# Optimization experiments

Measured on AMD Instinct MI355X. Metric: run time of the kernel, lower is better.

The kernel has to match this reference:

```python
import jax, jax.numpy as jnp
import numpy as np

T, B, E, H, F = 1024, 2, 1024, 16, 8
D = E // H
R = 2 * T - 1  # relative positions T-1 .. -(T-1)


def setup_inputs() -> dict:
    key = jax.random.key(0)
    ks = jax.random.split(key, 11)
    std = float(np.sqrt(2.0 / (E + E)))
    return {
        "input": jax.random.normal(ks[0], (T, B, E), jnp.float32),
        "pos": jax.random.normal(ks[1], (R, B, E), jnp.float32),
        "factor": jax.random.normal(ks[2], (F,), jnp.float32),
        "in_proj_weight": jax.random.normal(ks[3], (3 * E * E, F), jnp.float32) * std,
        "pos_proj_weight": jax.random.normal(ks[4], (E * E, F), jnp.float32) * std,
        "out_proj_weight": jax.random.normal(ks[5], (E * E, F), jnp.float32) * std,
        "in_proj_bias": jax.random.normal(ks[6], (3 * E, F), jnp.float32) * 0.02,
        "pos_proj_bias": jax.random.normal(ks[7], (E, F), jnp.float32) * 0.02,
        "out_proj_bias": jax.random.normal(ks[8], (E, F), jnp.float32) * 0.02,
        "r_w_bias": jax.random.normal(ks[9], (E, F), jnp.float32) * 0.02,
        "r_r_bias": jax.random.normal(ks[10], (E, F), jnp.float32) * 0.02,
    }


def _rel_shift(x):
    # x: [BH, T, R] -> out[b, i, j] = x[b, i, j + (T-1) - i]
    bh, q, r = x.shape
    zp = jnp.zeros((bh, q, 1), x.dtype)
    xp = jnp.concatenate([zp, x], axis=2).reshape(bh, r + 1, q)
    return xp[:, 1:, :].reshape(bh, q, r)


def reference(input, pos, factor, in_proj_weight, pos_proj_weight, out_proj_weight,
              in_proj_bias, pos_proj_bias, out_proj_bias, r_w_bias, r_r_bias):
    # hypernetwork: generate effective weights from factor vector (torch.mv)
    W_in = (in_proj_weight @ factor).reshape(3 * E, E)
    W_pos = (pos_proj_weight @ factor).reshape(E, E)
    W_out = (out_proj_weight @ factor).reshape(E, E)
    b_in = in_proj_bias @ factor
    b_pos = pos_proj_bias @ factor
    b_out = out_proj_bias @ factor
    rw = (r_w_bias @ factor).reshape(H, D)  # content bias
    rr = (r_r_bias @ factor).reshape(H, D)  # position bias

    qkv = input @ W_in.T + b_in                      # [T, B, 3E]
    q, k, v = jnp.split(qkv, 3, axis=-1)
    q = q.reshape(T, B, H, D)
    k = k.reshape(T, B, H, D)
    v = v.reshape(T, B, H, D)
    r = (pos @ W_pos.T + b_pos).reshape(R, B, H, D)  # [R, B, H, D]

    scale = 1.0 / np.sqrt(D)
    # AC: content-content + content bias term
    AC = jnp.einsum('ibhd,jbhd->bhij', q + rw, k)    # [B, H, T, T]
    # BD: content-position + position bias term, then relative shift
    BD = jnp.einsum('ibhd,rbhd->bhir', q + rr, r)    # [B, H, T, R]
    BD = _rel_shift(BD.reshape(B * H, T, R))[:, :, :T].reshape(B, H, T, T)

    attn = jax.nn.softmax((AC + BD) * scale, axis=-1)  # [B, H, T, T]
    out = jnp.einsum('bhij,jbhd->ibhd', attn, v).reshape(T, B, E)
    out = out @ W_out.T + b_out                       # [T, B, E]
    return out
```

## Files before the change

kernel.cpp:

```cpp
#include <hip/hip_runtime.h>


typedef _Float16 h16;
typedef _Float16 h16x8 __attribute__((ext_vector_type(8)));
typedef _Float16 h16x4 __attribute__((ext_vector_type(4)));
typedef float f32x4 __attribute__((ext_vector_type(4)));

static __device__ __forceinline__ f32x4 mfma16(h16x8 a, h16x8 b, f32x4 c) {
  return __builtin_amdgcn_mfma_f32_16x16x32_f16(a, b, c, 0, 0, 0);
}
static __device__ __forceinline__ void gload16(const void* g, void* l) {
  __builtin_amdgcn_global_load_lds((const __attribute__((address_space(1))) void*)g,
                                   (__attribute__((address_space(3))) void*)l, 16, 0, 0);
}

__global__ __launch_bounds__(256) void hypernet_kernel(
    const float* __restrict__ fac,
    const float* __restrict__ w_in, const float* __restrict__ w_pos,
    const float* __restrict__ w_out, const float* __restrict__ b_in_w,
    const float* __restrict__ b_pos_w, const float* __restrict__ b_out_w,
    const float* __restrict__ rw_w, const float* __restrict__ rr_w,
    h16* __restrict__ Win, h16* __restrict__ Wpos, h16* __restrict__ Wout,
    float* __restrict__ bin, float* __restrict__ bpos, float* __restrict__ bout,
    float* __restrict__ rw, float* __restrict__ rr, h16* __restrict__ rb,
    const float* __restrict__ input, h16* __restrict__ in_h,
    const float* __restrict__ pos, h16* __restrict__ pos_h)
{
  float f0=fac[0],f1=fac[1],f2=fac[2],f3=fac[3],f4=fac[4],f5=fac[5],f6=fac[6],f7=fac[7];
#define DOT8(p) ((p)[0]*f0+(p)[1]*f1+(p)[2]*f2+(p)[3]*f3+(p)[4]*f4+(p)[5]*f5+(p)[6]*f6+(p)[7]*f7)
  if (blockIdx.x < 5120) {
    const int lane = threadIdx.x & 63;
    const int gw = blockIdx.x * 4 + (threadIdx.x >> 6);
    size_t rowBase = (size_t)gw * 256;
    const float* srcp; h16* dstp; size_t lr;
    if (rowBase < 3145728)      { srcp = w_in;  dstp = Win;  lr = rowBase; }
    else if (rowBase < 4194304) { srcp = w_pos; dstp = Wpos; lr = rowBase - 3145728; }
    else                        { srcp = w_out; dstp = Wout; lr = rowBase - 4194304; }
    const f32x4* p = reinterpret_cast<const f32x4*>(srcp) + lr*2;
    const int pi = (lane < 32) ? (lane << 1) : (((lane - 32) << 1) | 1);
    const float fa = (lane < 32) ? f0 : f4;
    const float fb = (lane < 32) ? f1 : f5;
    const float fc = (lane < 32) ? f2 : f6;
    const float fd = (lane < 32) ? f3 : f7;
    f32x4 v[8];
#pragma unroll
    for (int u = 0; u < 8; ++u) v[u] = p[(size_t)u*64 + pi];
    __builtin_amdgcn_sched_barrier(0);
    float full[8];
#pragma unroll
    for (int u = 0; u < 8; ++u) {
      float part = v[u].x*fa + v[u].y*fb + v[u].z*fc + v[u].w*fd;
      full[u] = part + __shfl_xor(part, 32, 64);
    }
    if (lane < 32) {
#pragma unroll
      for (int u = 0; u < 8; ++u)
        dstp[lr + u*32 + lane] = (h16)full[u];
    }
    return;
  }
  int idx = (blockIdx.x - 5120) * 256 + threadIdx.x;
  if (idx < 3072) { bin[idx]  = DOT8(b_in_w  + (size_t)idx*8); return; }
  idx -= 3072;
  if (idx < 1024) { bpos[idx] = DOT8(b_pos_w + (size_t)idx*8); return; }
  idx -= 1024;
  if (idx < 1024) { bout[idx] = DOT8(b_out_w + (size_t)idx*8); return; }
  idx -= 1024;
  if (idx < 1024) { rw[idx]   = DOT8(rw_w    + (size_t)idx*8); return; }
  idx -= 1024;
  if (idx < 1024) { rr[idx]   = DOT8(rr_w    + (size_t)idx*8); return; }
  idx -= 1024;
  if (idx < 2048) { rb[(((size_t)(idx >> 6)) << 17) + 2047*64 + (idx & 63)] = (h16)0.f; return; }
  idx -= 2048;
  if (idx < 262144) {
    const float4* ip = reinterpret_cast<const float4*>(input) + (size_t)idx*2;
    float4 a = ip[0], b = ip[1];
    h16x8 o = { (h16)a.x, (h16)a.y, (h16)a.z, (h16)a.w,
                (h16)b.x, (h16)b.y, (h16)b.z, (h16)b.w };
    reinterpret_cast<h16x8*>(in_h)[idx] = o;
    return;
  }
  idx -= 262144;
  if (idx < 524032) {
    const float4* pp = reinterpret_cast<const float4*>(pos) + (size_t)idx*2;
    float4 a = pp[0], b = pp[1];
    h16x8 o = { (h16)a.x, (h16)a.y, (h16)a.z, (h16)a.w,
                (h16)b.x, (h16)b.y, (h16)b.z, (h16)b.w };
    reinterpret_cast<h16x8*>(pos_h)[idx] = o;
  }
#undef DOT8
}

__global__ __launch_bounds__(256) void gemm01_kernel(
    const h16* __restrict__ A0, const h16* __restrict__ B0, const float* __restrict__ bias0,
    const h16* __restrict__ A1, const h16* __restrict__ B1, const float* __restrict__ bias1,
    const float* __restrict__ rwv, const float* __restrict__ rrv,
    h16* __restrict__ o0, h16* __restrict__ o1,
    h16* __restrict__ o2, h16* __restrict__ o3, h16* __restrict__ r_out)
{
  __shared__ __align__(16) h16 a_sm[128*64];
  __shared__ __align__(16) h16 b_sm[128*64];
  const int bx = blockIdx.x;
  const int swz = (bx & 7) * 80 + (bx >> 3);
  int mode, bxx, byy;
  if (swz < 384) { mode = 0; bxx = swz % 24; byy = swz / 24; }
  else           { mode = 1; int b = swz - 384; bxx = b & 7; byy = b >> 3; }
  const h16* __restrict__ A  = mode ? A1 : A0;
  const h16* __restrict__ Bw = mode ? B1 : B0;
  const float* __restrict__ bias = mode ? bias1 : bias0;
  const int M = mode ? 4094 : 2048;
  const int K = 1024;

  const int tid = threadIdx.x, lane = tid & 63, wave = tid >> 6;
  const int quad = lane >> 4, t16 = lane & 15;
  const int wm = wave >> 1, wn = wave & 1;
  const int m0 = byy * 128, n0 = bxx * 128;
  const int lrow = lane >> 3, lgran = lane & 7;
  const int gsw = (lgran ^ lrow) * 8;
  const int xg0 = (quad ^ (t16 & 7)) * 8;
  const int xg1 = xg0 ^ 32;

  f32x4 acc[4][4];
#pragma unroll
  for (int i = 0; i < 4; ++i)
#pragma unroll
    for (int j = 0; j < 4; ++j) acc[i][j] = (f32x4){0.f,0.f,0.f,0.f};

  for (int k0 = 0; k0 < K; k0 += 64) {
    __syncthreads();
#pragma unroll
    for (int s = 0; s < 4; ++s) {
      int rbase = wave*32 + s*8;
      gload16(A  + (size_t)(m0 + rbase + lrow)*K + k0 + gsw, a_sm + rbase*64);
      gload16(Bw + (size_t)(n0 + rbase + lrow)*K + k0 + gsw, b_sm + rbase*64);
    }
    __syncthreads();
#pragma unroll
    for (int kc = 0; kc < 2; ++kc) {
      const int xg = kc ? xg1 : xg0;
      h16x8 af[4], bfr[4];
#pragma unroll
      for (int i = 0; i < 4; ++i) {
        af[i]  = *reinterpret_cast<const h16x8*>(a_sm + (wm*64 + i*16 + t16)*64 + xg);
        bfr[i] = *reinterpret_cast<const h16x8*>(b_sm + (wn*64 + i*16 + t16)*64 + xg);
      }
#pragma unroll
      for (int i = 0; i < 4; ++i)
#pragma unroll
        for (int j = 0; j < 4; ++j)
          acc[i][j] = mfma16(af[i], bfr[j], acc[i][j]);
    }
  }

#pragma unroll
  for (int i = 0; i < 4; ++i) {
    int mb = m0 + wm*64 + i*16 + quad*4;
#pragma unroll
    for (int j = 0; j < 4; ++j) {
      int n = n0 + wn*64 + j*16 + t16;
      float bv = bias[n];
      if (mode == 0) {
        int nn = n & 1023, sec = n >> 10, hh = nn >> 6, d = nn & 63;
        float rwb = rwv[nn], rrb = rrv[nn];
#pragma unroll
        for (int r = 0; r < 4; ++r) {
          int m = mb + r, t = m >> 1, b = m & 1;
          size_t off = ((size_t)((b << 4) + hh) << 16) + (t << 6) + d;
          float v = acc[i][j][r] + bv;
          if (sec == 0)      { o0[off] = (h16)(v + rwb); o1[off] = (h16)(v + rrb); }
          else if (sec == 1) { o2[off] = (h16)v; }
          else               { o3[off] = (h16)v; }
        }
      } else {
        int hh = n >> 6, d = n & 63;
#pragma unroll
        for (int r = 0; r < 4; ++r) {
          int m = mb + r;
          if (m < M) {
            int rel = m >> 1, b = m & 1;
            r_out[(((size_t)((b << 4) + hh)) << 17) + (rel << 6) + d] = (h16)(acc[i][j][r] + bv);
          }
        }
      }
    }
  }
}

template <int MODE>
__global__ __launch_bounds__(256) void gemm_lds_kernel(
    const h16* __restrict__ A, const h16* __restrict__ Bw,
    const float* __restrict__ bias, int M, int N, int K,
    float* __restrict__ Cout)
{
  __shared__ __align__(16) h16 a_sm[128*64];
  __shared__ __align__(16) h16 b_sm[128*64];
  const int tid = threadIdx.x, lane = tid & 63, wave = tid >> 6;
  const int quad = lane >> 4, t16 = lane & 15;
  const int wm = wave >> 1, wn = wave & 1;
  const int m0 = blockIdx.y * 128, n0 = blockIdx.x * 128;
  const int lrow = lane >> 3, lgran = lane & 7;
  const int gsw = (lgran ^ lrow) * 8;
  const int xg0 = (quad ^ (t16 & 7)) * 8;
  const int xg1 = xg0 ^ 32;

  f32x4 acc[4][4];
#pragma unroll
  for (int i = 0; i < 4; ++i)
#pragma unroll
    for (int j = 0; j < 4; ++j) acc[i][j] = (f32x4){0.f,0.f,0.f,0.f};

  for (int k0 = 0; k0 < K; k0 += 64) {
    __syncthreads();
#pragma unroll
    for (int s = 0; s < 4; ++s) {
      int rbase = wave*32 + s*8;
      gload16(A  + (size_t)(m0 + rbase + lrow)*K + k0 + gsw, a_sm + rbase*64);
      gload16(Bw + (size_t)(n0 + rbase + lrow)*K + k0 + gsw, b_sm + rbase*64);
    }
    __syncthreads();
#pragma unroll
    for (int kc = 0; kc < 2; ++kc) {
      const int xg = kc ? xg1 : xg0;
      h16x8 af[4], bfr[4];
#pragma unroll
      for (int i = 0; i < 4; ++i) {
        af[i]  = *reinterpret_cast<const h16x8*>(a_sm + (wm*64 + i*16 + t16)*64 + xg);
        bfr[i] = *reinterpret_cast<const h16x8*>(b_sm + (wn*64 + i*16 + t16)*64 + xg);
      }
#pragma unroll
      for (int i = 0; i < 4; ++i)
#pragma unroll
        for (int j = 0; j < 4; ++j)
          acc[i][j] = mfma16(af[i], bfr[j], acc[i][j]);
    }
  }

#pragma unroll
  for (int i = 0; i < 4; ++i) {
    int mb = m0 + wm*64 + i*16 + quad*4;
#pragma unroll
    for (int j = 0; j < 4; ++j) {
      int n = n0 + wn*64 + j*16 + t16;
      float bv = bias[n];
#pragma unroll
      for (int r = 0; r < 4; ++r)
        Cout[(size_t)(mb + r)*N + n] = acc[i][j][r] + bv;
    }
  }
}

__global__ __launch_bounds__(256) void transpose_v_kernel(
    const h16* __restrict__ vb, h16* __restrict__ vbt)
{
  __shared__ h16 tile[64*72];
  const int bh = blockIdx.y, t0 = blockIdx.x * 64;
  const int r = threadIdx.x >> 3, c = (threadIdx.x & 7) * 8;
  const h16* src = vb + ((size_t)bh << 16) + (size_t)(t0 + r)*64 + c;
  *reinterpret_cast<h16x8*>(tile + r*72 + c)        = *reinterpret_cast<const h16x8*>(src);
  *reinterpret_cast<h16x8*>(tile + (r + 32)*72 + c) = *reinterpret_cast<const h16x8*>(src + 32*64);
  __syncthreads();
  h16x8 o0, o1;
#pragma unroll
  for (int e = 0; e < 8; ++e) {
    o0[e] = tile[(c + e)*72 + r];
    o1[e] = tile[(c + e)*72 + r + 32];
  }
  h16* dst = vbt + ((size_t)bh << 16) + (size_t)r*1024 + t0 + c;
  *reinterpret_cast<h16x8*>(dst)            = o0;
  *reinterpret_cast<h16x8*>(dst + 32*1024)  = o1;
}

__global__ __launch_bounds__(256) void flash_kernel(
    const h16* __restrict__ qrw, const h16* __restrict__ qrr,
    const h16* __restrict__ kb, const h16* __restrict__ vbt,
    const h16* __restrict__ rb,
    float* __restrict__ o_part, float* __restrict__ ml_part)
{
  __shared__ __align__(16) h16 k_sm[64*64];
  __shared__ __align__(16) h16 vt_sm[64*64];
  __shared__ __align__(16) h16 r_sm[128*64];

  const int tid = threadIdx.x, lane = tid & 63, wave = tid >> 6;
  const int quad = lane >> 4, t16 = lane & 15;
  const int bh = blockIdx.y, i0 = blockIdx.x * 64, jh = blockIdx.z;
  const size_t base  = (size_t)bh << 16;
  const size_t rbase = (size_t)bh << 17;
  const int iw = i0 + wave * 16;
  const int lrow = lane >> 3, lgran = lane & 7;
  const int gsw = (lgran ^ lrow) * 8;
  const int xg0 = (quad ^ (t16 & 7)) * 8;
  const int xg1 = xg0 ^ 32;

  h16x8 a_rw[2], a_rr[2];
  {
    const h16* p = qrw + base + (size_t)(iw + t16)*64 + quad*8;
    a_rw[0] = *reinterpret_cast<const h16x8*>(p);
    a_rw[1] = *reinterpret_cast<const h16x8*>(p + 32);
    const h16* p2 = qrr + base + (size_t)(iw + t16)*64 + quad*8;
    a_rr[0] = *reinterpret_cast<const h16x8*>(p2);
    a_rr[1] = *reinterpret_cast<const h16x8*>(p2 + 32);
  }

  f32x4 o_acc[4];
#pragma unroll
  for (int dc = 0; dc < 4; ++dc) o_acc[dc] = (f32x4){0.f,0.f,0.f,0.f};
  float m_run[4] = {-1e30f,-1e30f,-1e30f,-1e30f};
  float l_run[4] = {0.f,0.f,0.f,0.f};

  h16* bdw = r_sm + wave * (16*84);
  const int cb0 = 3 - wave;

  for (int j0 = jh*512; j0 < jh*512 + 512; j0 += 64) {
    __syncthreads();
    {
#pragma unroll
      for (int s = 0; s < 2; ++s) {
        int row = wave*16 + s*8;
        gload16(kb  + base + (size_t)(j0 + row + lrow)*64 + gsw, k_sm  + row*64);
        gload16(vbt + base + (size_t)(row + lrow)*1024 + j0 + gsw, vt_sm + row*64);
      }
      const int rel0 = j0 - i0 + 960;
#pragma unroll
      for (int s = 0; s < 4; ++s) {
        int row = wave*32 + s*8;
        gload16(rb + rbase + (size_t)(rel0 + row + lrow)*64 + gsw, r_sm + row*64);
      }
    }
    __syncthreads();

    f32x4 s_ac[4];
#pragma unroll
    for (int c = 0; c < 4; ++c) {
      s_ac[c] = (f32x4){0.f,0.f,0.f,0.f};
      s_ac[c] = mfma16(a_rw[0], *reinterpret_cast<const h16x8*>(k_sm + (c*16 + t16)*64 + xg0), s_ac[c]);
      s_ac[c] = mfma16(a_rw[1], *reinterpret_cast<const h16x8*>(k_sm + (c*16 + t16)*64 + xg1), s_ac[c]);
    }
    f32x4 s_bd[5];
#pragma unroll
    for (int u = 0; u < 5; ++u) {
      s_bd[u] = (f32x4){0.f,0.f,0.f,0.f};
      s_bd[u] = mfma16(a_rr[0], *reinterpret_cast<const h16x8*>(r_sm + ((cb0+u)*16 + t16)*64 + xg0), s_bd[u]);
      s_bd[u] = mfma16(a_rr[1], *reinterpret_cast<const h16x8*>(r_sm + ((cb0+u)*16 + t16)*64 + xg1), s_bd[u]);
    }
    __syncthreads();

#pragma unroll
    for (int u = 0; u < 5; ++u)
#pragma unroll
      for (int r = 0; r < 4; ++r)
        bdw[(quad*4 + r)*84 + u*16 + t16] = (h16)s_bd[u][r];

    float sv[4][4];
#pragma unroll
    for (int c = 0; c < 4; ++c)
#pragma unroll
      for (int r = 0; r < 4; ++r) {
        int il = quad*4 + r;
        float bdv = (float)bdw[il*84 + c*16 + t16 + 15 - il];
        sv[c][r] = (s_ac[c][r] + bdv) * 0.125f;
      }

    float alpha[4];
#pragma unroll
    for (int r = 0; r < 4; ++r) {
      float v = fmaxf(fmaxf(sv[0][r], sv[1][r]), fmaxf(sv[2][r], sv[3][r]));
#pragma unroll
      for (int off = 1; off < 16; off <<= 1) v = fmaxf(v, __shfl_xor(v, off, 64));
      float mn = fmaxf(m_run[r], v);
      alpha[r] = __expf(m_run[r] - mn);
      m_run[r] = mn;
    }
#pragma unroll
    for (int r = 0; r < 4; ++r) {
      float s0 = 0.f;
#pragma unroll
      for (int c = 0; c < 4; ++c) {
        float p = __expf(sv[c][r] - m_run[r]);
        sv[c][r] = p; s0 += p;
      }
      l_run[r] = l_run[r]*alpha[r] + s0;
    }
#pragma unroll
    for (int dc = 0; dc < 4; ++dc) {
      f32x4 t = o_acc[dc];
#pragma unroll
      for (int r = 0; r < 4; ++r) t[r] *= alpha[r];
      o_acc[dc] = t;
    }
    h16* pw = bdw;
#pragma unroll
    for (int c = 0; c < 4; ++c)
#pragma unroll
      for (int r = 0; r < 4; ++r)
        pw[(quad*4 + r)*72 + c*16 + t16] = (h16)sv[c][r];

    h16x8 ap0 = *reinterpret_cast<const h16x8*>(pw + t16*72 + quad*8);
    h16x8 ap1 = *reinterpret_cast<const h16x8*>(pw + t16*72 + 32 + quad*8);
#pragma unroll
    for (int dc = 0; dc < 4; ++dc) {
      h16x8 bv0 = *reinterpret_cast<const h16x8*>(vt_sm + (dc*16 + t16)*64 + xg0);
      h16x8 bv1 = *reinterpret_cast<const h16x8*>(vt_sm + (dc*16 + t16)*64 + xg1);
      o_acc[dc] = mfma16(ap0, bv0, o_acc[dc]);
      o_acc[dc] = mfma16(ap1, bv1, o_acc[dc]);
    }
  }

#pragma unroll
  for (int r = 0; r < 4; ++r) {
    float l = l_run[r];
#pragma unroll
    for (int off = 1; off < 16; off <<= 1) l += __shfl_xor(l, off, 64);
    l_run[r] = l;
  }
  const size_t obase = ((size_t)jh*32 + bh) * 1024 * 64;
#pragma unroll
  for (int r = 0; r < 4; ++r) {
    int i = iw + quad*4 + r;
#pragma unroll
    for (int dc = 0; dc < 4; ++dc)
      o_part[obase + (size_t)i*64 + dc*16 + t16] = o_acc[dc][r];
    if (t16 == 0) {
      size_t mo = (((size_t)jh*32 + bh)*1024 + i)*2;
      ml_part[mo]     = m_run[r];
      ml_part[mo + 1] = l_run[r];
    }
  }
}

__global__ __launch_bounds__(256) void combine_kernel(
    const float* __restrict__ o_part, const float* __restrict__ ml_part,
    h16* __restrict__ attn_h)
{
  int gid = blockIdx.x * 256 + threadIdx.x;
  int row = gid >> 4;
  int d4 = (gid & 15) * 4;
  float m[2], l[2];
#pragma unroll
  for (int p = 0; p < 2; ++p) {
    m[p] = ml_part[p*65536 + row*2];
    l[p] = ml_part[p*65536 + row*2 + 1];
  }
  float M = fmaxf(m[0], m[1]);
  float e[2], den = 0.f;
#pragma unroll
  for (int p = 0; p < 2; ++p) { e[p] = __expf(m[p] - M); den += e[p]*l[p]; }
  float inv = 1.f / den;
  float4 acc = {0.f,0.f,0.f,0.f};
#pragma unroll
  for (int p = 0; p < 2; ++p) {
    float4 O = *reinterpret_cast<const float4*>(o_part + (size_t)p*2097152 + (size_t)row*64 + d4);
    acc.x += e[p]*O.x; acc.y += e[p]*O.y; acc.z += e[p]*O.z; acc.w += e[p]*O.w;
  }
  int bh = row >> 10, i = row & 1023, b = bh >> 4, h = bh & 15;
  h16x4 o = { (h16)(acc.x*inv), (h16)(acc.y*inv), (h16)(acc.z*inv), (h16)(acc.w*inv) };
  *reinterpret_cast<h16x4*>(attn_h + ((size_t)(i*2 + b))*1024 + h*64 + d4) = o;
}

extern "C" void kernel_launch(void* const* d_in, const int* in_sizes, int n_in,
                              void* d_out, int out_size, void* d_ws, size_t ws_size,
                              hipStream_t stream)
{
  const float* input  = (const float*)d_in[0];
  const float* pos    = (const float*)d_in[1];
  const float* fac    = (const float*)d_in[2];
  const float* w_in   = (const float*)d_in[3];
  const float* w_pos  = (const float*)d_in[4];
  const float* w_out  = (const float*)d_in[5];
  const float* bin_w  = (const float*)d_in[6];
  const float* bpos_w = (const float*)d_in[7];
  const float* bout_w = (const float*)d_in[8];
  const float* rw_w   = (const float*)d_in[9];
  const float* rr_w   = (const float*)d_in[10];
  float* out = (float*)d_out;
  (void)in_sizes; (void)n_in; (void)out_size; (void)ws_size;

  char* w = (char*)d_ws;
  auto take = [&](size_t bytes) { char* p = w; w += bytes; return p; };
  h16*   Win    = (h16*)take(3145728ull*2);
  h16*   Wpos   = (h16*)take(1048576ull*2);
  h16*   Wout   = (h16*)take(1048576ull*2);
  float* bin    = (float*)take(3072*4);
  float* bpos   = (float*)take(1024*4);
  float* bout   = (float*)take(1024*4);
  float* rw     = (float*)take(1024*4);
  float* rr     = (float*)take(1024*4);
  h16*   in_h   = (h16*)take(2097152ull*2);
  h16*   pos_h  = (h16*)take(4192256ull*2);
  h16*   qrwb   = (h16*)take(2097152ull*2);
  h16*   qrrb   = (h16*)take(2097152ull*2);
  h16*   kb     = (h16*)take(2097152ull*2);
  h16*   vb     = (h16*)take(2097152ull*2);
  h16*   vbt    = (h16*)take(2097152ull*2);
  h16*   rb     = (h16*)take(4194304ull*2);
  float* o_part = (float*)take(4ull*2097152ull*4);
  float* ml     = (float*)take(4ull*65536ull*4);
  h16*   attn_h = (h16*)take(2097152ull*2);

  hypernet_kernel<<<8227, 256, 0, stream>>>(fac, w_in, w_pos, w_out, bin_w, bpos_w, bout_w,
                                            rw_w, rr_w, Win, Wpos, Wout, bin, bpos, bout,
                                            rw, rr, rb, input, in_h, pos, pos_h);
  gemm01_kernel<<<640, 256, 0, stream>>>(in_h, Win, bin, pos_h, Wpos, bpos,
                                         rw, rr, qrwb, qrrb, kb, vb, rb);
  transpose_v_kernel<<<dim3(16, 32), 256, 0, stream>>>(vb, vbt);
  flash_kernel<<<dim3(16, 32, 2), 256, 0, stream>>>(qrwb, qrrb, kb, vbt, rb, o_part, ml);
  combine_kernel<<<2048, 256, 0, stream>>>(o_part, ml, attn_h);
  gemm_lds_kernel<2><<<dim3(8, 16), 256, 0, stream>>>(attn_h, Wout, bout, 2048, 1024, 1024,
                                                      out);
}
```

Measured before the change: 354.2 us.

## Drop split-K flash attention and combine kernel; normalize output in flash epilogue

The flash attention kernel no longer splits the key range across two blocks. Each block now iterates over all 1024 keys and writes the normalized fp16 output directly, so the separate combine kernel and the fp32 partial-output buffers are removed. This cuts a launch and the partial-result traffic, but halves the grid to 512 blocks, which may leave CUs underused on a large GPU. A sched_barrier in the hypernet kernel is also removed, and the output GEMM template is renamed.

Result: no change. 351.7 us (-0.7%).

```diff
diff --git a/kernel.cpp b/kernel.cpp
--- a/kernel.cpp
+++ b/kernel.cpp
@@ -45,7 +45,6 @@
     f32x4 v[8];
 #pragma unroll
     for (int u = 0; u < 8; ++u) v[u] = p[(size_t)u*64 + pi];
-    __builtin_amdgcn_sched_barrier(0);
     float full[8];
 #pragma unroll
     for (int u = 0; u < 8; ++u) {
@@ -186,8 +185,7 @@
   }
 }
 
-template <int MODE>
-__global__ __launch_bounds__(256) void gemm_lds_kernel(
+__global__ __launch_bounds__(256) void gemm2_kernel(
     const h16* __restrict__ A, const h16* __restrict__ Bw,
     const float* __restrict__ bias, int M, int N, int K,
     float* __restrict__ Cout)
@@ -274,7 +272,7 @@
     const h16* __restrict__ qrw, const h16* __restrict__ qrr,
     const h16* __restrict__ kb, const h16* __restrict__ vbt,
     const h16* __restrict__ rb,
-    float* __restrict__ o_part, float* __restrict__ ml_part)
+    h16* __restrict__ attn_h)
 {
   __shared__ __align__(16) h16 k_sm[64*64];
   __shared__ __align__(16) h16 vt_sm[64*64];
@@ -282,7 +280,7 @@
 
   const int tid = threadIdx.x, lane = tid & 63, wave = tid >> 6;
   const int quad = lane >> 4, t16 = lane & 15;
-  const int bh = blockIdx.y, i0 = blockIdx.x * 64, jh = blockIdx.z;
+  const int bh = blockIdx.y, i0 = blockIdx.x * 64;
   const size_t base  = (size_t)bh << 16;
   const size_t rbase = (size_t)bh << 17;
   const int iw = i0 + wave * 16;
@@ -310,7 +308,7 @@
   h16* bdw = r_sm + wave * (16*84);
   const int cb0 = 3 - wave;
 
-  for (int j0 = jh*512; j0 < jh*512 + 512; j0 += 64) {
+  for (int j0 = 0; j0 < 1024; j0 += 64) {
     __syncthreads();
     {
 #pragma unroll
@@ -405,55 +403,19 @@
     }
   }
 
+  const int b = bh >> 4, hh = bh & 15;
 #pragma unroll
   for (int r = 0; r < 4; ++r) {
     float l = l_run[r];
 #pragma unroll
     for (int off = 1; off < 16; off <<= 1) l += __shfl_xor(l, off, 64);
-    l_run[r] = l;
-  }
-  const size_t obase = ((size_t)jh*32 + bh) * 1024 * 64;
-#pragma unroll
-  for (int r = 0; r < 4; ++r) {
+    float inv = 1.f / l;
     int i = iw + quad*4 + r;
+    h16* dst = attn_h + ((size_t)(i*2 + b))*1024 + hh*64;
 #pragma unroll
     for (int dc = 0; dc < 4; ++dc)
-      o_part[obase + (size_t)i*64 + dc*16 + t16] = o_acc[dc][r];
-    if (t16 == 0) {
-      size_t mo = (((size_t)jh*32 + bh)*1024 + i)*2;
-      ml_part[mo]     = m_run[r];
-      ml_part[mo + 1] = l_run[r];
-    }
-  }
-}
-
-__global__ __launch_bounds__(256) void combine_kernel(
-    const float* __restrict__ o_part, const float* __restrict__ ml_part,
-    h16* __restrict__ attn_h)
-{
-  int gid = blockIdx.x * 256 + threadIdx.x;
-  int row = gid >> 4;
-  int d4 = (gid & 15) * 4;
-  float m[2], l[2];
-#pragma unroll
-  for (int p = 0; p < 2; ++p) {
-    m[p] = ml_part[p*65536 + row*2];
-    l[p] = ml_part[p*65536 + row*2 + 1];
-  }
-  float M = fmaxf(m[0], m[1]);
-  float e[2], den = 0.f;
-#pragma unroll
-  for (int p = 0; p < 2; ++p) { e[p] = __expf(m[p] - M); den += e[p]*l[p]; }
-  float inv = 1.f / den;
-  float4 acc = {0.f,0.f,0.f,0.f};
-#pragma unroll
-  for (int p = 0; p < 2; ++p) {
-    float4 O = *reinterpret_cast<const float4*>(o_part + (size_t)p*2097152 + (size_t)row*64 + d4);
-    acc.x += e[p]*O.x; acc.y += e[p]*O.y; acc.z += e[p]*O.z; acc.w += e[p]*O.w;
-  }
-  int bh = row >> 10, i = row & 1023, b = bh >> 4, h = bh & 15;
-  h16x4 o = { (h16)(acc.x*inv), (h16)(acc.y*inv), (h16)(acc.z*inv), (h16)(acc.w*inv) };
-  *reinterpret_cast<h16x4*>(attn_h + ((size_t)(i*2 + b))*1024 + h*64 + d4) = o;
+      dst[dc*16 + t16] = (h16)(o_acc[dc][r] * inv);
+  }
 }
 
 extern "C" void kernel_launch(void* const* d_in, const int* in_sizes, int n_in,
@@ -492,8 +454,6 @@
   h16*   vb     = (h16*)take(2097152ull*2);
   h16*   vbt    = (h16*)take(2097152ull*2);
   h16*   rb     = (h16*)take(4194304ull*2);
-  float* o_part = (float*)take(4ull*2097152ull*4);
-  float* ml     = (float*)take(4ull*65536ull*4);
   h16*   attn_h = (h16*)take(2097152ull*2);
 
   hypernet_kernel<<<8227, 256, 0, stream>>>(fac, w_in, w_pos, w_out, bin_w, bpos_w, bout_w,
@@ -502,8 +462,7 @@
   gemm01_kernel<<<640, 256, 0, stream>>>(in_h, Win, bin, pos_h, Wpos, bpos,
                                          rw, rr, qrwb, qrrb, kb, vb, rb);
   transpose_v_kernel<<<dim3(16, 32), 256, 0, stream>>>(vb, vbt);
-  flash_kernel<<<dim3(16, 32, 2), 256, 0, stream>>>(qrwb, qrrb, kb, vbt, rb, o_part, ml);
-  combine_kernel<<<2048, 256, 0, stream>>>(o_part, ml, attn_h);
-  gemm_lds_kernel<2><<<dim3(8, 16), 256, 0, stream>>>(attn_h, Wout, bout, 2048, 1024, 1024,
-                                                      out);
-}
+  flash_kernel<<<dim3(16, 32), 256, 0, stream>>>(qrwb, qrrb, kb, vbt, rb, attn_h);
+  gemm2_kernel<<<dim3(8, 16), 256, 0, stream>>>(attn_h, Wout, bout, 2048, 1024, 1024,
+                                                out);
+}
```
